# Optimization experiments

Hardware: AMD Instinct MI355X
Metric: run time of the kernel (lower is better)

The kernel has to match this reference:

```python
import jax, jax.numpy as jnp
import numpy as np

HEADS = 8
DIM_HEAD = 64
SCALE = DIM_HEAD ** -0.5


def setup_inputs() -> dict:
    key = jax.random.key(0)
    ks = jax.random.split(key, 6)
    b, n, d = 2, 4096, 1024
    inner = HEADS * DIM_HEAD  # 512
    x = jax.random.normal(ks[0], (b, n, d), dtype=jnp.float32)
    Wq = jax.random.normal(ks[1], (d, inner), dtype=jnp.float32) * (d ** -0.5)
    Wk = jax.random.normal(ks[2], (d, inner), dtype=jnp.float32) * (d ** -0.5)
    Wv = jax.random.normal(ks[3], (d, inner), dtype=jnp.float32) * (d ** -0.5)
    Wout = jax.random.normal(ks[4], (inner, d), dtype=jnp.float32) * (inner ** -0.5)
    bout = jnp.zeros((d,), dtype=jnp.float32)
    return {"x": x, "Wq": Wq, "Wk": Wk, "Wv": Wv, "Wout": Wout, "bout": bout}


def reference(x, Wq, Wk, Wv, Wout, bout):
    b, n, _ = x.shape
    h, dh = HEADS, DIM_HEAD
    # self-attention: context = x
    q = (x @ Wq).reshape(b, n, h, dh).transpose(0, 2, 1, 3)  # b h n d
    k = (x @ Wk).reshape(b, n, h, dh).transpose(0, 2, 1, 3)
    v = (x @ Wv).reshape(b, n, h, dh).transpose(0, 2, 1, 3)
    sim = jnp.einsum('bhid,bhjd->bhij', q, k) * SCALE  # full score matrix
    attn = jax.nn.softmax(sim, axis=-1)
    out = jnp.einsum('bhij,bhjd->bhid', attn, v)
    out = out.transpose(0, 2, 1, 3).reshape(b, n, h * dh)  # b n (h d)
    return out @ Wout + bout
```

## Files before the change

### kernel.cpp

```cpp
#include <hip/hip_runtime.h>
#include <hip/hip_bf16.h>

typedef __bf16 bf16x8 __attribute__((ext_vector_type(8)));
typedef __bf16 bf16x4 __attribute__((ext_vector_type(4)));
typedef float floatx4 __attribute__((ext_vector_type(4)));

#define MFMA16(a, b, c) __builtin_amdgcn_mfma_f32_16x16x32_bf16((a), (b), (c), 0, 0, 0)

__device__ __forceinline__ void stage16(const __bf16* g, __bf16* lds_base) {
  __builtin_amdgcn_global_load_lds(
      (__attribute__((address_space(1))) void*)(void*)g,
      (__attribute__((address_space(3))) void*)lds_base, 16, 0, 0);
}

__global__ void detect_dtype(const unsigned int* __restrict__ x, int* __restrict__ flag) {
  __shared__ int cnt;
  if (threadIdx.x == 0) cnt = 0;
  __syncthreads();
  int c = 0;
  for (int i = threadIdx.x; i < 4096; i += 256) {
    const unsigned f = (x[i] >> 7) & 0xFF;
    c += (f >= 100 && f <= 140) ? 1 : 0;
  }
  atomicAdd(&cnt, c);
  __syncthreads();
  if (threadIdx.x == 0) *flag = (cnt > 2048) ? 1 : 0;
}

__global__ __launch_bounds__(256) void convert_x(const void* __restrict__ src,
                                                 __bf16* __restrict__ dst,
                                                 const int* __restrict__ flagp) {
  const int isbf = *flagp;
  const size_t i = ((size_t)blockIdx.x * 256 + threadIdx.x) * 8;
  if (isbf) {
    *(bf16x8*)(dst + i) = *(const bf16x8*)((const __bf16*)src + i);
  } else {
    const float4 f0 = *(const float4*)((const float*)src + i);
    const float4 f1 = *(const float4*)((const float*)src + i + 4);
    bf16x8 v;
    v[0] = (__bf16)f0.x; v[1] = (__bf16)f0.y; v[2] = (__bf16)f0.z; v[3] = (__bf16)f0.w;
    v[4] = (__bf16)f1.x; v[5] = (__bf16)f1.y; v[6] = (__bf16)f1.z; v[7] = (__bf16)f1.w;
    *(bf16x8*)(dst + i) = v;
  }
}

__global__ __launch_bounds__(256) void transpose3_conv(
    const void* __restrict__ s0, const void* __restrict__ s1,
    const void* __restrict__ s2, __bf16* __restrict__ dst,
    int R, int C, const int* __restrict__ flagp) {
  __shared__ __bf16 t[32][33];
  const int isbf = *flagp;
  const void* src = (blockIdx.z == 0) ? s0 : (blockIdx.z == 1) ? s1 : s2;
  __bf16* d = dst + (size_t)blockIdx.z * R * C;
  const int bx = blockIdx.x * 32, by = blockIdx.y * 32;
  const int x = threadIdx.x & 31, y0 = threadIdx.x >> 5;
#pragma unroll
  for (int i = y0; i < 32; i += 8) {
    const size_t idx = (size_t)(by + i) * C + bx + x;
    t[i][x] = isbf ? ((const __bf16*)src)[idx] : (__bf16)(((const float*)src)[idx]);
  }
  __syncthreads();
#pragma unroll
  for (int i = y0; i < 32; i += 8) d[(size_t)(bx + i) * R + by + x] = t[x][i];
}

__global__ __launch_bounds__(256) void transpose_conv(const void* __restrict__ src,
                                                      __bf16* __restrict__ dst,
                                                      int R, int C,
                                                      const int* __restrict__ flagp) {
  __shared__ __bf16 t[32][33];
  const int isbf = *flagp;
  const int bx = blockIdx.x * 32, by = blockIdx.y * 32;
  const int x = threadIdx.x & 31, y0 = threadIdx.x >> 5;
#pragma unroll
  for (int i = y0; i < 32; i += 8) {
    const size_t idx = (size_t)(by + i) * C + bx + x;
    t[i][x] = isbf ? ((const __bf16*)src)[idx] : (__bf16)(((const float*)src)[idx]);
  }
  __syncthreads();
#pragma unroll
  for (int i = y0; i < 32; i += 8) dst[(size_t)(bx + i) * R + by + x] = t[x][i];
}

__global__ __launch_bounds__(256) void vp_transpose(const __bf16* __restrict__ V,
                                                    __bf16* __restrict__ VP) {
  alignas(16) __shared__ __bf16 t[64][64];
  const int bh = blockIdx.y, s0 = blockIdx.x * 64;
  const int row = threadIdx.x >> 2, part = threadIdx.x & 3;
  const __bf16* src = V + (size_t)bh * 262144 + (size_t)(s0 + row) * 64 + part * 16;
  *(bf16x8*)&t[row][part * 16] = *(const bf16x8*)src;
  *(bf16x8*)&t[row][part * 16 + 8] = *(const bf16x8*)(src + 8);
  __syncthreads();
  const int d = row, og = part;
  bf16x8 w0, w1;
#pragma unroll
  for (int e = 0; e < 8; e++) {
    const int o0 = og * 16 + e, o1 = og * 16 + 8 + e;
    w0[e] = t[(o0 & 3) * 16 + (o0 >> 2)][d];
    w1[e] = t[(o1 & 3) * 16 + (o1 >> 2)][d];
  }
  __bf16* dst = VP + (size_t)bh * 262144 + (size_t)d * 4096 + s0 + og * 16;
  *(bf16x8*)dst = w0;
  *(bf16x8*)(dst + 8) = w1;
}

__global__ __launch_bounds__(256) void gemm_bt(
    const __bf16* __restrict__ A, const __bf16* __restrict__ Bt,
    void* __restrict__ Cv, void* __restrict__ Cv2, int M, int N, int K,
    const void* __restrict__ bias, int permute, int egress_dual,
    size_t zsB, size_t zsC, const int* __restrict__ flagp) {
  alignas(16) __shared__ __bf16 As[2][128 * 32];
  alignas(16) __shared__ __bf16 Bs[2][128 * 32];
  const int isbf = *flagp;
  Bt += blockIdx.z * zsB;
  const size_t zoff = (size_t)blockIdx.z * zsC;
  const int tid = threadIdx.x;
  const int wave = tid >> 6, lane = tid & 63;
  const int m0 = blockIdx.y * 128, n0 = blockIdx.x * 128;
  const int wm = (wave & 1) * 64, wn = (wave >> 1) * 64;
  const int fr = lane & 15, fq = lane >> 4;

  const floatx4 zero4 = {0.f, 0.f, 0.f, 0.f};
  floatx4 acc[4][4];
#pragma unroll
  for (int i = 0; i < 4; i++)
#pragma unroll
    for (int j = 0; j < 4; j++) acc[i][j] = zero4;

  const int lrow = lane >> 2;
  const int lk = (lane & 3) * 8;
  const int NT = K >> 5;

#pragma unroll
  for (int cc = 0; cc < 2; ++cc) {
    const int c = 2 * wave + cc;
    stage16(A + (size_t)(m0 + c * 16 + lrow) * K + lk, &As[0][c * 512]);
    stage16(Bt + (size_t)(n0 + c * 16 + lrow) * K + lk, &Bs[0][c * 512]);
  }

  for (int t = 0; t < NT; ++t) {
    const int cur = t & 1;
    if (t + 1 < NT) {
      const int k1 = (t + 1) << 5;
#pragma unroll
      for (int cc = 0; cc < 2; ++cc) {
        const int c = 2 * wave + cc;
        stage16(A + (size_t)(m0 + c * 16 + lrow) * K + k1 + lk, &As[1 - cur][c * 512]);
        stage16(Bt + (size_t)(n0 + c * 16 + lrow) * K + k1 + lk, &Bs[1 - cur][c * 512]);
      }
      asm volatile("s_waitcnt vmcnt(4)" ::: "memory");
    } else {
      asm volatile("s_waitcnt vmcnt(0)" ::: "memory");
    }
    __builtin_amdgcn_s_barrier();
    __builtin_amdgcn_sched_barrier(0);
    bf16x8 af[4], bg[4];
#pragma unroll
    for (int mt = 0; mt < 4; mt++)
      af[mt] = *(const bf16x8*)&As[cur][(wm + mt * 16 + fr) * 32 + fq * 8];
#pragma unroll
    for (int nt = 0; nt < 4; nt++)
      bg[nt] = *(const bf16x8*)&Bs[cur][(wn + nt * 16 + fr) * 32 + fq * 8];
#pragma unroll
    for (int mt = 0; mt < 4; mt++)
#pragma unroll
      for (int nt = 0; nt < 4; nt++)
        acc[mt][nt] = MFMA16(af[mt], bg[nt], acc[mt][nt]);
    __builtin_amdgcn_sched_barrier(0);
    __builtin_amdgcn_s_barrier();
  }

  const float qs = (permute && blockIdx.z == 0) ? 0.18033688011112042f
                                                : 1.0f;
#pragma unroll
  for (int mt = 0; mt < 4; mt++)
#pragma unroll
    for (int nt = 0; nt < 4; nt++)
#pragma unroll
      for (int r = 0; r < 4; r++) {
        const int row = m0 + wm + mt * 16 + fq * 4 + r;
        const int col = n0 + wn + nt * 16 + fr;
        float v = acc[mt][nt][r] * qs;
        if (bias)
          v += isbf ? (float)((const __bf16*)bias)[col] : ((const float*)bias)[col];
        if (permute) {
          const int bh = (row >> 12) * 8 + (col >> 6);
          const int s = row & 4095, d = col & 63;
          const size_t pidx = (size_t)bh * 262144 + (size_t)s * 64 + d;
          if (blockIdx.z == 2)
            ((__bf16*)Cv2)[pidx] = (__bf16)v;
          else
            ((__bf16*)Cv)[zoff + pidx] = (__bf16)v;
        } else {
          const size_t idx = (size_t)row * N + col;
          if (egress_dual && !isbf)
            ((float*)Cv)[idx] = v;
          else
            ((__bf16*)Cv)[idx] = (__bf16)v;
        }
      }
}

#define ATT_S 4096
__global__ __launch_bounds__(512, 4) void attn_flash(
    const __bf16* __restrict__ Qa, const __bf16* __restrict__ Ka,
    const __bf16* __restrict__ VPa, __bf16* __restrict__ O) {
  alignas(16) __shared__ __bf16 Kl[2][64 * 64];
  alignas(16) __shared__ __bf16 Vl[2][64 * 64];
  alignas(16) __shared__ __bf16 Pl[8 * 32 * 64];
  const int tid = threadIdx.x, wave = tid >> 6, lane = tid & 63;
  const int bh = blockIdx.y, b = bh >> 3, h = bh & 7;
  const int q0 = blockIdx.x * 256 + wave * 32;
  const int fr = lane & 15, fq = lane >> 4;
  const __bf16* Qb = Qa + (size_t)bh * ATT_S * 64;
  const __bf16* Kb = Ka + (size_t)bh * ATT_S * 64;
  const __bf16* Vb = VPa + (size_t)bh * ATT_S * 64;

  const int sw0 = ((fq ^ (fr & 7)) * 8);
  const int sw1 = (((fq + 4) ^ (fr & 7)) * 8);
  const int r0 = tid >> 3;
  const int ssw = (((tid & 7) ^ (r0 & 7)) * 8);

  bf16x8 aq[2][2];
#pragma unroll
  for (int mt = 0; mt < 2; mt++)
#pragma unroll
    for (int kt = 0; kt < 2; kt++)
      aq[mt][kt] = *(const bf16x8*)(Qb + (size_t)(q0 + mt * 16 + fr) * 64 + kt * 32 + fq * 8);

  const floatx4 zero4 = {0.f, 0.f, 0.f, 0.f};
  floatx4 o[2][4];
  float lsum[2][4];
#pragma unroll
  for (int mt = 0; mt < 2; mt++) {
#pragma unroll
    for (int nt = 0; nt < 4; nt++) o[mt][nt] = zero4;
#pragma unroll
    for (int r = 0; r < 4; r++) lsum[mt][r] = 0.f;
  }

  const int JT = ATT_S / 64;

  stage16(Kb + (size_t)r0 * 64 + ssw, &Kl[0][wave * 512]);
  stage16(Vb + (size_t)r0 * 4096 + ssw, &Vl[0][wave * 512]);

  for (int j = 0; j < JT; ++j) {
    __syncthreads();
    const int cur = j & 1;
    if (j + 1 < JT) {
      const int kv1 = (j + 1) * 64;
      stage16(Kb + (size_t)(kv1 + r0) * 64 + ssw, &Kl[1 - cur][wave * 512]);
      stage16(Vb + (size_t)r0 * 4096 + kv1 + ssw, &Vl[1 - cur][wave * 512]);
    }
    const __bf16* Klc = Kl[cur];
    const __bf16* Vlc = Vl[cur];

    floatx4 s4[2][4];
    __builtin_amdgcn_s_setprio(1);
#pragma unroll
    for (int nt = 0; nt < 4; nt++) {
      bf16x8 bk0 = *(const bf16x8*)&Klc[(nt * 16 + fr) * 64 + sw0];
      bf16x8 bk1 = *(const bf16x8*)&Klc[(nt * 16 + fr) * 64 + sw1];
#pragma unroll
      for (int mt = 0; mt < 2; mt++) {
        floatx4 zz = zero4;
        zz = MFMA16(aq[mt][0], bk0, zz);
        zz = MFMA16(aq[mt][1], bk1, zz);
        s4[mt][nt] = zz;
      }
    }
    __builtin_amdgcn_s_setprio(0);

#pragma unroll
    for (int mt = 0; mt < 2; mt++)
#pragma unroll
      for (int r = 0; r < 4; r++) {
        bf16x4 pv;
        float psum = 0.f;
#pragma unroll
        for (int nt = 0; nt < 4; nt++) {
          const float p = __builtin_amdgcn_exp2f(s4[mt][nt][r]);
          pv[nt] = (__bf16)p;
          psum += p;
        }
        lsum[mt][r] += psum;
        const int row = wave * 32 + mt * 16 + fq * 4 + r;
        const int vg = (fr >> 1) ^ ((fq * 4 + r) & 7);
        *(bf16x4*)&Pl[row * 64 + vg * 8 + (fr & 1) * 4] = pv;
      }
    asm volatile("s_waitcnt lgkmcnt(0)" ::: "memory");

    bf16x8 bv[4][2];
#pragma unroll
    for (int nt = 0; nt < 4; nt++) {
      bv[nt][0] = *(const bf16x8*)&Vlc[(nt * 16 + fr) * 64 + sw0];
      bv[nt][1] = *(const bf16x8*)&Vlc[(nt * 16 + fr) * 64 + sw1];
    }
    __builtin_amdgcn_s_setprio(1);
#pragma unroll
    for (int mt = 0; mt < 2; mt++) {
      const int prow = (wave * 32 + mt * 16 + fr) * 64;
      bf16x8 ap0 = *(const bf16x8*)&Pl[prow + sw0];
      bf16x8 ap1 = *(const bf16x8*)&Pl[prow + sw1];
#pragma unroll
      for (int nt = 0; nt < 4; nt++) {
        o[mt][nt] = MFMA16(ap0, bv[nt][0], o[mt][nt]);
        o[mt][nt] = MFMA16(ap1, bv[nt][1], o[mt][nt]);
      }
    }
    __builtin_amdgcn_s_setprio(0);
  }

#pragma unroll
  for (int off = 1; off < 16; off <<= 1)
#pragma unroll
    for (int mt = 0; mt < 2; mt++)
#pragma unroll
      for (int r = 0; r < 4; r++) lsum[mt][r] += __shfl_xor(lsum[mt][r], off, 64);

#pragma unroll
  for (int mt = 0; mt < 2; mt++)
#pragma unroll
    for (int r = 0; r < 4; r++) {
      const float inv = 1.0f / lsum[mt][r];
      const int row = q0 + mt * 16 + fq * 4 + r;
      __bf16* Orow = O + (size_t)(b * ATT_S + row) * 512 + h * 64;
#pragma unroll
      for (int nt = 0; nt < 4; nt++)
        Orow[nt * 16 + fr] = (__bf16)(o[mt][nt][r] * inv);
    }
}

extern "C" void kernel_launch(void* const* d_in, const int* in_sizes, int n_in,
                              void* d_out, int out_size, void* d_ws, size_t ws_size,
                              hipStream_t stream) {
  (void)in_sizes; (void)n_in; (void)out_size; (void)ws_size;
  const void* x = d_in[0];
  const void* Wq = d_in[1];
  const void* Wk = d_in[2];
  const void* Wv = d_in[3];
  const void* Wout = d_in[4];
  const void* bout = d_in[5];

  char* ws = (char*)d_ws;
  int* flag = (int*)ws;
  __bf16* wtq = (__bf16*)(ws + (1u << 20));
  __bf16* wto = (__bf16*)(ws + (4u << 20));
  __bf16* Q = (__bf16*)(ws + (5u << 20));
  __bf16* K = (__bf16*)(ws + (13u << 20));
  __bf16* VP = (__bf16*)(ws + (21u << 20));
  __bf16* O = (__bf16*)(ws + (29u << 20));
  __bf16* Vtmp = O;
  __bf16* xbf = (__bf16*)(ws + (38u << 20));

  detect_dtype<<<1, 256, 0, stream>>>((const unsigned int*)x, flag);

  transpose3_conv<<<dim3(16, 32, 3), 256, 0, stream>>>(Wq, Wk, Wv, wtq, 1024, 512, flag);
  transpose_conv<<<dim3(32, 16), 256, 0, stream>>>(Wout, wto, 512, 1024, flag);

  convert_x<<<4096, 256, 0, stream>>>(x, xbf, flag);

  gemm_bt<<<dim3(4, 64, 3), 256, 0, stream>>>(
      xbf, wtq, Q, Vtmp, 8192, 512, 1024, nullptr, 1, 0,
      (size_t)512 * 1024, (size_t)8192 * 512, flag);

  vp_transpose<<<dim3(64, 16), 256, 0, stream>>>(Vtmp, VP);

  attn_flash<<<dim3(ATT_S / 256, 16), 512, 0, stream>>>(Q, K, VP, O);

  gemm_bt<<<dim3(8, 64, 1), 256, 0, stream>>>(
      O, wto, d_out, nullptr, 8192, 1024, 512, bout, 0, 1, 0, 0, flag);
}
```

Baseline: 264.9 us.

## Triple-buffer K/V in flash attention with smaller 256-thread blocks

The attention kernel changes from 512-thread blocks covering 256 queries to 256-thread blocks covering 128 queries, so each thread now issues two 16-byte async loads per K and V tile. K/V staging moves from double to triple buffering, prefetching two tiles ahead. Explicit vmcnt waits plus barriers at the start and end of each iteration replace the single __syncthreads. The goal is to hide global-load latency behind the MFMA work, at the cost of more LDS per block, an extra barrier per iteration, and twice as many blocks that each reload K/V.

```diff
diff --git a/kernel.cpp b/kernel.cpp
--- a/kernel.cpp
+++ b/kernel.cpp
@@ -202,15 +202,15 @@
 }
 
 #define ATT_S 4096
-__global__ __launch_bounds__(512, 4) void attn_flash(
+__global__ __launch_bounds__(256, 2) void attn_flash(
     const __bf16* __restrict__ Qa, const __bf16* __restrict__ Ka,
     const __bf16* __restrict__ VPa, __bf16* __restrict__ O) {
-  alignas(16) __shared__ __bf16 Kl[2][64 * 64];
-  alignas(16) __shared__ __bf16 Vl[2][64 * 64];
-  alignas(16) __shared__ __bf16 Pl[8 * 32 * 64];
+  alignas(16) __shared__ __bf16 Kl[3][64 * 64];
+  alignas(16) __shared__ __bf16 Vl[3][64 * 64];
+  alignas(16) __shared__ __bf16 Pl[4 * 32 * 64];
   const int tid = threadIdx.x, wave = tid >> 6, lane = tid & 63;
   const int bh = blockIdx.y, b = bh >> 3, h = bh & 7;
-  const int q0 = blockIdx.x * 256 + wave * 32;
+  const int q0 = blockIdx.x * 128 + wave * 32;
   const int fr = lane & 15, fq = lane >> 4;
   const __bf16* Qb = Qa + (size_t)bh * ATT_S * 64;
   const __bf16* Kb = Ka + (size_t)bh * ATT_S * 64;
@@ -241,17 +241,32 @@
 
   const int JT = ATT_S / 64;
 
-  stage16(Kb + (size_t)r0 * 64 + ssw, &Kl[0][wave * 512]);
-  stage16(Vb + (size_t)r0 * 4096 + ssw, &Vl[0][wave * 512]);
+#pragma unroll
+  for (int t0 = 0; t0 < 2; ++t0) {
+    const int kv = t0 * 64;
+    stage16(Kb + (size_t)(kv + r0) * 64 + ssw, &Kl[t0][wave * 512]);
+    stage16(Kb + (size_t)(kv + 32 + r0) * 64 + ssw, &Kl[t0][2048 + wave * 512]);
+    stage16(Vb + (size_t)r0 * 4096 + kv + ssw, &Vl[t0][wave * 512]);
+    stage16(Vb + (size_t)(32 + r0) * 4096 + kv + ssw, &Vl[t0][2048 + wave * 512]);
+  }
 
   for (int j = 0; j < JT; ++j) {
-    __syncthreads();
-    const int cur = j & 1;
-    if (j + 1 < JT) {
-      const int kv1 = (j + 1) * 64;
-      stage16(Kb + (size_t)(kv1 + r0) * 64 + ssw, &Kl[1 - cur][wave * 512]);
-      stage16(Vb + (size_t)r0 * 4096 + kv1 + ssw, &Vl[1 - cur][wave * 512]);
-    }
+    const int cur = j % 3;
+    if (j + 2 < JT) {
+      const int sl = (j + 2) % 3;
+      const int kv2 = (j + 2) * 64;
+      stage16(Kb + (size_t)(kv2 + r0) * 64 + ssw, &Kl[sl][wave * 512]);
+      stage16(Kb + (size_t)(kv2 + 32 + r0) * 64 + ssw, &Kl[sl][2048 + wave * 512]);
+      stage16(Vb + (size_t)r0 * 4096 + kv2 + ssw, &Vl[sl][wave * 512]);
+      stage16(Vb + (size_t)(32 + r0) * 4096 + kv2 + ssw, &Vl[sl][2048 + wave * 512]);
+      asm volatile("s_waitcnt vmcnt(8)" ::: "memory");
+    } else if (j + 1 < JT) {
+      asm volatile("s_waitcnt vmcnt(4)" ::: "memory");
+    } else {
+      asm volatile("s_waitcnt vmcnt(0)" ::: "memory");
+    }
+    __builtin_amdgcn_s_barrier();
+    __builtin_amdgcn_sched_barrier(0);
     const __bf16* Klc = Kl[cur];
     const __bf16* Vlc = Vl[cur];
 
@@ -309,6 +324,8 @@
       }
     }
     __builtin_amdgcn_s_setprio(0);
+    __builtin_amdgcn_sched_barrier(0);
+    __builtin_amdgcn_s_barrier();
   }
 
 #pragma unroll
@@ -366,7 +383,7 @@
 
   vp_transpose<<<dim3(64, 16), 256, 0, stream>>>(Vtmp, VP);
 
-  attn_flash<<<dim3(ATT_S / 256, 16), 512, 0, stream>>>(Q, K, VP, O);
+  attn_flash<<<dim3(ATT_S / 128, 16), 256, 0, stream>>>(Q, K, VP, O);
 
   gemm_bt<<<dim3(8, 64, 1), 256, 0, stream>>>(
       O, wto, d_out, nullptr, 8192, 1024, 512, bout, 0, 1, 0, 0, flag);
```

After: 260.6 us. About the same (-1.6%).
